# Performance work log

Hardware: AMD Instinct MI355X
Metric: run time of the kernel (lower is better)

The kernel has to match this reference:

```python
import jax, jax.numpy as jnp
import numpy as np
from jax import lax

B, L, D = 8, 2048, 512
K = 16            # cysteines per sequence (fixed by construction)
CYS = 4           # AA2ID['C']
CW = 5            # disulfide_context_window
KW = 2 * CW + 1   # conv kernel size = 11
H = D // 2        # LSTM hidden per direction = 256
STR = 0.4         # cys_optimization_strength


def setup_inputs() -> dict:
    key = jax.random.key(0)
    ks = jax.random.split(key, 16)
    hidden_states = jax.random.normal(ks[0], (B, L, D), jnp.float32)
    # amino-acid ids with exactly K cysteines per sequence, spaced > KW apart
    aa = jax.random.randint(ks[1], (B, L), 0, 20)
    aa = jnp.where(aa == CYS, 5, aa)
    base = 64 + 128 * jnp.arange(K)
    jitter = jax.random.randint(ks[2], (B, K), -40, 41)
    pos = base[None, :] + jitter  # [B,K], strictly increasing, gaps > 11
    aa_ids = aa.at[jnp.arange(B)[:, None], pos].set(CYS)
    s = 0.05
    W_bil = jax.random.normal(ks[3], (128, D, D)) * s
    b_bil = jax.random.normal(ks[4], (128,)) * s
    cls_w1 = jax.random.normal(ks[5], (64, 128)) * s
    cls_b1 = jax.random.normal(ks[6], (64,)) * s
    cls_w2 = jax.random.normal(ks[7], (1, 64)) * s
    cls_b2 = jax.random.normal(ks[8], (1,)) * s
    # 2 layers x 2 directions; both layers have input size D (2*H == D)
    lstm_Wih = jax.random.normal(ks[9], (2, 2, 4 * H, D)) * s
    lstm_Whh = jax.random.normal(ks[10], (2, 2, 4 * H, H)) * s
    lstm_bih = jax.random.normal(ks[11], (2, 2, 4 * H)) * s
    lstm_bhh = jax.random.normal(ks[12], (2, 2, 4 * H)) * s
    conv_w = jax.random.normal(ks[13], (D, D, KW)) * 0.02
    conv_b = jax.random.normal(ks[14], (D,)) * 0.02
    dsb_factor = jax.random.normal(ks[15], (D,)) * 0.1
    return dict(hidden_states=hidden_states, aa_ids=aa_ids, W_bil=W_bil,
                b_bil=b_bil, cls_w1=cls_w1, cls_b1=cls_b1, cls_w2=cls_w2,
                cls_b2=cls_b2, lstm_Wih=lstm_Wih, lstm_Whh=lstm_Whh,
                lstm_bih=lstm_bih, lstm_bhh=lstm_bhh, conv_w=conv_w,
                conv_b=conv_b, dsb_factor=dsb_factor)


def _lstm_dir(x, Wih, Whh, bih, bhh, reverse):
    # x: [B,L,In] -> [B,L,H]; PyTorch gate order i,f,g,o
    bsz = x.shape[0]
    xs = jnp.swapaxes(x, 0, 1)  # [L,B,In]
    if reverse:
        xs = xs[::-1]

    def step(carry, xt):
        h, c = carry
        g = xt @ Wih.T + h @ Whh.T + bih + bhh  # [B,4H]
        i, f, gg, o = jnp.split(g, 4, axis=-1)
        c = jax.nn.sigmoid(f) * c + jax.nn.sigmoid(i) * jnp.tanh(gg)
        h = jax.nn.sigmoid(o) * jnp.tanh(c)
        return (h, c), h

    init = (jnp.zeros((bsz, H), x.dtype), jnp.zeros((bsz, H), x.dtype))
    _, hs = lax.scan(step, init, xs)
    if reverse:
        hs = hs[::-1]
    return jnp.swapaxes(hs, 0, 1)


def _bilstm(x, Wih, Whh, bih, bhh):
    out = x
    for layer in range(2):  # dropout inactive in eval mode
        fw = _lstm_dir(out, Wih[layer, 0], Whh[layer, 0], bih[layer, 0], bhh[layer, 0], False)
        bw = _lstm_dir(out, Wih[layer, 1], Whh[layer, 1], bih[layer, 1], bhh[layer, 1], True)
        out = jnp.concatenate([fw, bw], axis=-1)
    return out


def reference(hidden_states, aa_ids, W_bil, b_bil, cls_w1, cls_b1, cls_w2,
              cls_b2, lstm_Wih, lstm_Whh, lstm_bih, lstm_bhh, conv_w, conv_b,
              dsb_factor):
    dt = hidden_states.dtype
    cys_mask = (aa_ids == CYS)  # [B,L] bool, exactly K per row
    pos = jax.vmap(lambda m: jnp.nonzero(m, size=K, fill_value=0)[0])(cys_mask)  # [B,K]

    # ---- batched bilinear + classifier over all cys pairs ----
    feats = jnp.take_along_axis(hidden_states, pos[:, :, None], axis=1)  # [B,K,D]
    t = jnp.einsum('bkd,cde->bkce', feats, W_bil)            # [B,K,128,D]
    pf = jnp.einsum('bkce,bme->bkmc', t, feats) + b_bil      # [B,K,K,128]
    h1 = jax.nn.relu(pf @ cls_w1.T + cls_b1)
    prob = jax.nn.sigmoid(h1 @ cls_w2.T + cls_b2)[..., 0]    # [B,K,K]
    dist = jnp.abs(pos[:, :, None] - pos[:, None, :])
    prob = jnp.where(dist < 2, prob * 0.1, prob)

    # ---- greedy NMS-style pair selection (prob desc, prob > 0.5, no reuse) ----
    iu, ju = jnp.triu_indices(K, k=1)  # P = K*(K-1)/2 pairs
    probs_flat = prob[:, iu, ju]       # [B,P]

    def greedy(pflat):
        order = jnp.argsort(-pflat)
        ii, jj, pp = iu[order], ju[order], pflat[order]

        def step(used, trip):
            i, j, p = trip
            sel = jnp.logical_and(jnp.logical_and(~used[i], ~used[j]), p > 0.5)
            used = used.at[i].set(used[i] | sel)
            used = used.at[j].set(used[j] | sel)
            return used, sel

        _, sels = lax.scan(step, jnp.zeros(K, bool), (ii, jj, pp))
        return jnp.zeros(iu.shape[0], bool).at[order].set(sels)

    sel_flat = jax.vmap(greedy)(probs_flat)
    sel_mat = jnp.zeros((B, K, K), bool).at[:, iu, ju].set(sel_flat)

    # ---- redox LSTM + windowed cys enhancement ----
    opt = _bilstm(hidden_states, lstm_Wih, lstm_Whh, lstm_bih, lstm_bhh)  # [B,L,D]
    cm = cys_mask.astype(dt)
    cov = lax.conv_general_dilated(cm[:, None, :], jnp.ones((1, 1, KW), dt),
                                   (1,), ((CW, CW),),
                                   dimension_numbers=('NCH', 'OIH', 'NCH'))[:, 0, :]
    win = (cov > 0).astype(dt)  # [B,L] 1 where within CW of a cysteine
    cys_enh = hidden_states + STR * opt * win[..., None] + dsb_factor * cm[..., None]

    # ---- local structure conv ----
    struct = lax.conv_general_dilated(jnp.swapaxes(cys_enh, 1, 2), conv_w,
                                      (1,), ((CW, CW),),
                                      dimension_numbers=('NCH', 'OIH', 'NCH'))
    struct = jnp.swapaxes(struct + conv_b[None, :, None], 1, 2)

    output = hidden_states + 0.3 * (cys_enh - hidden_states) + 0.2 * (struct - hidden_states)
    return (output, prob, sel_mat)
```

## Files before the change

### kernel.cpp

```cpp
#include <hip/hip_runtime.h>
#include <hip/hip_bf16.h>

typedef float  f32x4 __attribute__((ext_vector_type(4)));
typedef float  f32x2 __attribute__((ext_vector_type(2)));
typedef int    i32x4 __attribute__((ext_vector_type(4)));
typedef int    i32x8 __attribute__((ext_vector_type(8)));

#define NB   8
#define LSEQ 2048
#define DDIM 512
#define KC   16

__device__ __forceinline__ float rcp_(float x){ return __builtin_amdgcn_rcpf(x); }
__device__ __forceinline__ float ex2_(float x){ return __builtin_amdgcn_exp2f(x); }
__device__ __forceinline__ float clamp60(float x){ return fminf(fmaxf(x, -60.f), 60.f); }
__device__ __forceinline__ unsigned pk2(float a, float b){
    __hip_bfloat16 x=__float2bfloat16(a), y=__float2bfloat16(b);
    return (unsigned)*(unsigned short*)&x | ((unsigned)*(unsigned short*)&y<<16);
}

#define GLDS(gp, lp) __builtin_amdgcn_global_load_lds(                      \
    (__attribute__((address_space(1))) const void*)(gp),                   \
    (__attribute__((address_space(3))) void*)(lp), 16, 0, 0)

__global__ __launch_bounds__(256) void k_prep(const float* __restrict__ hidden, __hip_bfloat16* __restrict__ hbf,
                                              const float* __restrict__ Wih, __hip_bfloat16* __restrict__ wihbf,
                                              const float* __restrict__ bih, const float* __restrict__ bhh,
                                              float* __restrict__ bias2,
                                              const float* __restrict__ convw, __hip_bfloat16* __restrict__ wtc,
                                              const int* __restrict__ aa, int* __restrict__ pos,
                                              float* __restrict__ cm, float* __restrict__ win){
    int bid = blockIdx.x, tid = threadIdx.x;
    if(bid < 4096){
        size_t i = (size_t)bid*256 + tid;
        const f32x4* s = (const f32x4*)(hidden + i*8);
        f32x4 v0 = s[0], v1 = s[1];
        i32x4 o; o.x = pk2(v0.x,v0.y); o.y = pk2(v0.z,v0.w);
                 o.z = pk2(v1.x,v1.y); o.w = pk2(v1.z,v1.w);
        ((i32x4*)hbf)[i] = o;
    } else if(bid < 5120){
        size_t i = (size_t)(bid-4096)*256 + tid;
        const f32x4* s = (const f32x4*)(Wih + i*8);
        f32x4 v0 = s[0], v1 = s[1];
        i32x4 o; o.x = pk2(v0.x,v0.y); o.y = pk2(v0.z,v0.w);
                 o.z = pk2(v1.x,v1.y); o.w = pk2(v1.z,v1.w);
        ((i32x4*)wihbf)[i] = o;
    } else if(bid < 5136){
        int i = (bid-5120)*256 + tid;
        bias2[i] = bih[i] + bhh[i];
    } else if(bid < 6160){
        int idx = (bid-5136)*256 + tid;
        #pragma unroll
        for(int tap=0; tap<11; ++tap)
            wtc[(size_t)tap*262144 + idx] = __float2bfloat16(convw[(size_t)idx*11 + tap]);
    } else {
        int b = bid - 6160;
        __shared__ unsigned char fl[LSEQ];
        for(int t=tid; t<LSEQ; t+=256) fl[t] = (aa[b*LSEQ+t]==4) ? 1 : 0;
        __syncthreads();
        if(tid==0){
            int c=0;
            for(int t=0; t<LSEQ && c<KC; ++t) if(fl[t]) pos[b*KC + c++] = t;
            for(; c<KC; ++c) pos[b*KC+c]=0;
        }
        for(int t=tid; t<LSEQ; t+=256){
            cm[b*LSEQ+t] = fl[t] ? 1.f : 0.f;
            int lo = t-5 < 0 ? 0 : t-5;
            int hi = t+5 > LSEQ-1 ? LSEQ-1 : t+5;
            float wv = 0.f;
            for(int u=lo; u<=hi; ++u) if(fl[u]) wv = 1.f;
            win[b*LSEQ+t] = wv;
        }
    }
}

__global__ __launch_bounds__(256) void k_gemm(const __hip_bfloat16* __restrict__ A, const __hip_bfloat16* __restrict__ Bw,
                                              const float* __restrict__ bias, __hip_bfloat16* __restrict__ C,
                                              int N, int KD){
    int nt = blockIdx.x, mt = blockIdx.y;
    __shared__ __hip_bfloat16 As[128][32];
    __shared__ __hip_bfloat16 Bs[128][32];
    int tid = threadIdx.x, w = tid>>6, lane = tid&63, lo = lane&15, hi = lane>>4;
    int wm = w>>1, wn = w&1;
    f32x4 acc[4][4];
    #pragma unroll
    for(int s=0;s<4;s++){
        #pragma unroll
        for(int t2=0;t2<4;t2++) acc[s][t2] = (f32x4){0.f,0.f,0.f,0.f};
    }
    int lr = lane>>2, lc = (lane&3)*8;
    const __hip_bfloat16* Ab = A  + (size_t)(mt*128)*KD;
    const __hip_bfloat16* Bb = Bw + (size_t)(nt*128)*KD;
    for(int kk=0; kk<KD; kk+=32){
        __builtin_amdgcn_s_barrier();
        GLDS(Ab + (size_t)(w*32    + lr)*KD + kk + lc, &As[w*32   ][0]);
        GLDS(Ab + (size_t)(w*32+16 + lr)*KD + kk + lc, &As[w*32+16][0]);
        GLDS(Bb + (size_t)(w*32    + lr)*KD + kk + lc, &Bs[w*32   ][0]);
        GLDS(Bb + (size_t)(w*32+16 + lr)*KD + kk + lc, &Bs[w*32+16][0]);
        asm volatile("s_waitcnt vmcnt(0)" ::: "memory");
        __builtin_amdgcn_s_barrier();
        i32x4 av[4], bv[4];
        #pragma unroll
        for(int s=0;s<4;s++) av[s] = *(const i32x4*)(&As[wm*64+s*16+lo][hi*8]);
        #pragma unroll
        for(int t2=0;t2<4;t2++) bv[t2] = *(const i32x4*)(&Bs[wn*64+t2*16+lo][hi*8]);
        asm volatile("s_nop 1" ::);
        #pragma unroll
        for(int s=0;s<4;s++){
            #pragma unroll
            for(int t2=0;t2<4;t2++)
                asm volatile("v_mfma_f32_16x16x32_bf16 %0, %1, %2, %0" : "+v"(acc[s][t2]) : "v"(av[s]), "v"(bv[t2]));
        }
    }
    asm volatile("s_nop 7\n\ts_nop 7" ::);
    #pragma unroll
    for(int t2=0;t2<4;t2++){
        int n = nt*128 + wn*64 + t2*16 + lo;
        float bn = bias[n];
        #pragma unroll
        for(int s=0;s<4;s++){
            #pragma unroll
            for(int rr=0;rr<4;rr++){
                int m = mt*128 + wm*64 + s*16 + hi*4 + rr;
                C[(size_t)m*N + n] = __float2bfloat16(acc[s][t2][rr] + bn);
            }
        }
    }
}

__device__ __forceinline__ void recur_body(char* smem, const float* __restrict__ Whh,
        const __hip_bfloat16* __restrict__ Gx, __hip_bfloat16* __restrict__ Hout,
        int layer, int bat, int dir){
    unsigned char (*hb)[256]   = (unsigned char(*)[256])smem;
    __hip_bfloat16 (*gxs)[1024] = (__hip_bfloat16(*)[1024])(smem+512);
    const int tid = threadIdx.x, w = tid>>6, lane = tid&63, lo = lane&15, hi = lane>>4;
    for(int i=tid; i<128; i+=512) ((int*)smem)[i] = 0;

    i32x8 bf[8][2];
    const float* wbase = Whh + ((size_t)(layer*2 + dir)*1024)*256;
    #pragma unroll
    for(int q=0;q<4;q++){
        #pragma unroll
        for(int s=0;s<2;s++){
            int j = q*256 + w*32 + s*16 + lo;
            const float* wr = wbase + (size_t)j*256;
            #pragma unroll
            for(int c=0;c<2;c++){
                i32x8 v;
                #pragma unroll
                for(int u=0; u<8; ++u){
                    f32x4 wv = *(const f32x4*)(wr + c*128 + hi*32 + u*4);
                    int pk = __builtin_amdgcn_cvt_pk_fp8_f32(wv.x, wv.y, 0, false);
                    pk = __builtin_amdgcn_cvt_pk_fp8_f32(wv.z, wv.w, pk, true);
                    v[u] = pk;
                }
                bf[q*2+s][c] = v;
            }
        }
    }
    const int pm = w*32 + ((hi&1)<<4) + lo;
    float cst = 0.f;
    const __hip_bfloat16* gxbase = Gx + (size_t)bat*LSEQ*2048 + dir*1024;

    {
        int tok0 = dir ? (LSEQ-1) : 0;
        int tok1 = dir ? (LSEQ-2) : 1;
        if(w < 2){
            GLDS(gxbase + (size_t)tok0*2048 + w*512 + lane*8, &gxs[0][w*512]);
            GLDS(gxbase + (size_t)tok1*2048 + w*512 + lane*8, &gxs[1][w*512]);
        }
    }
    asm volatile("s_waitcnt vmcnt(1) lgkmcnt(0)" ::: "memory");
    __builtin_amdgcn_s_barrier();
    __builtin_amdgcn_sched_barrier(0);

    int cur = 0;
    for(int t=0; t<LSEQ; ++t){
        const int tt = dir ? (LSEQ-1-t) : t;
        const int hcur = t&1, hnxt = hcur^1;
        int nx2 = cur+2; if(nx2>=3) nx2-=3;
        {
            int tp = (t+2 < LSEQ) ? (t+2) : (LSEQ-1);
            int tok = dir ? (LSEQ-1-tp) : tp;
            if(w < 2) GLDS(gxbase + (size_t)tok*2048 + w*512 + lane*8, &gxs[nx2][w*512]);
        }
        i32x8 af[2];
        #pragma unroll
        for(int c=0;c<2;c++){
            i32x4 v0 = *(const i32x4*)(&hb[hcur][c*128 + hi*32]);
            i32x4 v1 = *(const i32x4*)(&hb[hcur][c*128 + hi*32 + 16]);
            af[c] = __builtin_shufflevector(v0, v1, 0,1,2,3,4,5,6,7);
        }
        f32x4 acc[8];
        #pragma unroll
        for(int i=0;i<8;i++) acc[i] = (f32x4){0.f,0.f,0.f,0.f};
        asm volatile("s_nop 1" ::);
        #pragma unroll
        for(int c=0;c<2;c++){
            #pragma unroll
            for(int i=0;i<8;i++)
                asm volatile("v_mfma_f32_16x16x128_f8f6f4 %0, %1, %2, %0"
                             : "+v"(acc[i]) : "v"(af[c]), "a"(bf[i][c]));
        }
        asm volatile("s_nop 7\n\ts_nop 7\n\ts_nop 7" ::);
        {
            float aI = (hi&1) ? acc[1][0] : acc[0][0];
            float aF = (hi&1) ? acc[3][0] : acc[2][0];
            float aG = (hi&1) ? acc[5][0] : acc[4][0];
            float aO = (hi&1) ? acc[7][0] : acc[6][0];
            float gi = aI + __bfloat162float(gxs[cur][      pm]);
            float gf = aF + __bfloat162float(gxs[cur][256 + pm]);
            float gg = aG + __bfloat162float(gxs[cur][512 + pm]);
            float go = aO + __bfloat162float(gxs[cur][768 + pm]);
            float sf = rcp_(1.f + ex2_(gf * -1.44269504f));
            float ag = ex2_(clamp60(gg * 2.88539008f));
            float bi = ex2_(clamp60(gi * -1.44269504f));
            float it = (ag - 1.f) * rcp_((1.f + bi) * (ag + 1.f));
            float c  = sf*cst + it;
            cst = c;
            float ac = ex2_(clamp60(c * 2.88539008f));
            float bo = ex2_(clamp60(go * -1.44269504f));
            float h  = (ac - 1.f) * rcp_((1.f + bo) * (ac + 1.f));
            if(hi < 2){
                int pk = __builtin_amdgcn_cvt_pk_fp8_f32(h, h, 0, false);
                hb[hnxt][pm] = (unsigned char)(pk & 0xff);
                Hout[((size_t)bat*LSEQ + tt)*512 + dir*256 + pm] = __float2bfloat16(h);
            }
        }
        asm volatile("s_waitcnt vmcnt(2) lgkmcnt(0)" ::: "memory");
        __builtin_amdgcn_s_barrier();
        __builtin_amdgcn_sched_barrier(0);
        cur = (cur+1 == 3) ? 0 : cur+1;
    }
}

__device__ __forceinline__ void bilinear_body(char* smem, const float* __restrict__ hidden,
        const int* __restrict__ pos, const float* __restrict__ Wb, const float* __restrict__ bb,
        float* __restrict__ pf, int idx){
    int c = idx & 127, b = idx >> 7;
    float (*fl)[516] = (float(*)[516])smem;
    float (*tl)[516] = (float(*)[516])(smem + 33024);
    int tid = threadIdx.x;
    for(int i=tid; i<2048; i+=512){
        int k = i>>7, d = (i&127)*4;
        int p = pos[b*KC + k];
        f32x4 v = *(const f32x4*)(hidden + ((size_t)b*LSEQ + p)*DDIM + d);
        fl[k][d]=v.x; fl[k][d+1]=v.y; fl[k][d+2]=v.z; fl[k][d+3]=v.w;
    }
    __syncthreads();
    int e = tid;
    float acc[16];
    #pragma unroll
    for(int k=0;k<16;k++) acc[k]=0.f;
    const float* wc = Wb + (size_t)c*512*512;
    for(int d=0; d<512; ++d){
        float wv = wc[(size_t)d*512 + e];
        #pragma unroll
        for(int k=0;k<16;k++) acc[k] += fl[k][d]*wv;
    }
    #pragma unroll
    for(int k=0;k<16;k++) tl[k][e] = acc[k];
    __syncthreads();
    if(tid < 256){
        int kq = tid>>4, mq = tid&15;
        const f32x4* tp = (const f32x4*)&tl[kq][0];
        const f32x4* fp = (const f32x4*)&fl[mq][0];
        float s = 0.f;
        #pragma unroll 8
        for(int e2=0;e2<128;e2++){ f32x4 a=tp[e2], v=fp[e2]; s += a.x*v.x + a.y*v.y + a.z*v.z + a.w*v.w; }
        pf[(((size_t)b*16+kq)*16+mq)*128 + c] = s + bb[c];
    }
}

__device__ __forceinline__ void clsgreedy_body(char* smem, const float* __restrict__ pf,
        const float* __restrict__ w1, const float* __restrict__ b1,
        const float* __restrict__ w2, const float* __restrict__ b2,
        const int* __restrict__ pos, float* __restrict__ prob, float* __restrict__ sel, int b){
    float (*sw1)[128] = (float(*)[128])smem;
    float* sw2 = (float*)(smem + 32768);
    float* sb1 = sw2 + 64;
    float* sp  = sb1 + 64;
    unsigned char* si = (unsigned char*)(sp + 120);
    unsigned char* sj = si + 120;
    int tid = threadIdx.x;
    for(int i=tid; i<8192; i+=512) sw1[i>>7][i&127] = w1[i];
    if(tid<64){ sw2[tid]=w2[tid]; sb1[tid]=b1[tid]; }
    if(tid==0){
        int idx=0;
        for(int i=0;i<16;i++) for(int j=i+1;j<16;j++){ si[idx]=(unsigned char)i; sj[idx]=(unsigned char)j; idx++; }
    }
    if(tid<256) sel[b*256+tid] = 0.f;
    __syncthreads();
    if(tid < 256){
        int k = tid>>4, m = tid&15;
        const f32x4* pp = (const f32x4*)(pf + (((size_t)b*16+k)*16+m)*128);
        f32x4 pr[32];
        #pragma unroll
        for(int i=0;i<32;i++) pr[i] = pp[i];
        float lg = b2[0];
        for(int n=0;n<64;n++){
            const f32x4* wr = (const f32x4*)&sw1[n][0];
            float a = sb1[n];
            #pragma unroll
            for(int i=0;i<32;i++){ f32x4 wv = wr[i]; a += pr[i].x*wv.x + pr[i].y*wv.y + pr[i].z*wv.z + pr[i].w*wv.w; }
            a = fmaxf(a, 0.f);
            lg += a*sw2[n];
        }
        float p = rcp_(1.f + ex2_(lg * -1.44269504f));
        int dk = pos[b*16+k]-pos[b*16+m]; if(dk<0) dk=-dk;
        if(dk<2) p *= 0.1f;
        prob[b*256 + k*16 + m] = p;
        if(k < m) sp[k*(31-k)/2 + (m-k-1)] = p;
    }
    __syncthreads();
    if(tid==0){
        bool done[120]; bool used[16];
        for(int i=0;i<120;i++) done[i]=false;
        for(int i=0;i<16;i++)  used[i]=false;
        for(int it=0; it<120; ++it){
            int bi=-1; float bp=-1e30f;
            for(int q=0;q<120;q++) if(!done[q] && sp[q]>bp){ bp=sp[q]; bi=q; }
            done[bi]=true;
            if(bp>0.5f && !used[si[bi]] && !used[sj[bi]]){
                used[si[bi]]=true; used[sj[bi]]=true;
                sel[b*256 + si[bi]*16 + sj[bi]] = 1.f;
            }
        }
    }
}

__global__ __launch_bounds__(512) void k_fused1(const float* __restrict__ Whh, const __hip_bfloat16* __restrict__ Gx,
        __hip_bfloat16* __restrict__ Hout,
        const float* __restrict__ hidden, const int* __restrict__ pos,
        const float* __restrict__ Wbil, const float* __restrict__ bbil, float* __restrict__ pf){
    __shared__ __attribute__((aligned(16))) char smem[98304];
    if(blockIdx.x < 16){
        recur_body(smem, Whh, Gx, Hout, 0, blockIdx.x>>1, blockIdx.x&1);
    } else {
        bilinear_body(smem, hidden, pos, Wbil, bbil, pf, blockIdx.x - 16);
    }
}

__global__ __launch_bounds__(512) void k_fused2(const float* __restrict__ Whh, const __hip_bfloat16* __restrict__ Gx,
        __hip_bfloat16* __restrict__ Hout,
        const float* __restrict__ pf, const float* __restrict__ w1, const float* __restrict__ b1,
        const float* __restrict__ w2, const float* __restrict__ b2, const int* __restrict__ pos,
        float* __restrict__ prob, float* __restrict__ sel){
    __shared__ __attribute__((aligned(16))) char smem[98304];
    if(blockIdx.x < 16){
        recur_body(smem, Whh, Gx, Hout, 1, blockIdx.x>>1, blockIdx.x&1);
    } else {
        clsgreedy_body(smem, pf, w1, b1, w2, b2, pos, prob, sel, blockIdx.x - 16);
    }
}

__global__ __launch_bounds__(256) void k_convce(const float* __restrict__ hs, const __hip_bfloat16* __restrict__ opt,
        const float* __restrict__ win, const float* __restrict__ cm, const float* __restrict__ dsb,
        const __hip_bfloat16* __restrict__ wt, const float* __restrict__ convb, float* __restrict__ outp){
    int mt = blockIdx.x & 31, b = blockIdx.x >> 5;
    __shared__ __hip_bfloat16 S[74][520];
    int tid = threadIdx.x;
    for(int i=tid; i<74*64; i+=256){
        int rq = i>>6, cc = (i&63)*8;
        int tok = mt*64 - 5 + rq;
        i32x4 o = (i32x4){0,0,0,0};
        if(tok>=0 && tok<LSEQ){
            size_t base = ((size_t)b*LSEQ + tok)*512 + cc;
            float wv = win[b*LSEQ+tok]*0.4f, cv = cm[b*LSEQ+tok];
            f32x4 h0 = *(const f32x4*)(hs + base);
            f32x4 h1 = *(const f32x4*)(hs + base + 4);
            unsigned long long u0 = *(const unsigned long long*)(opt + base);
            unsigned long long u1 = *(const unsigned long long*)(opt + base + 4);
            f32x4 d0 = *(const f32x4*)(dsb + cc);
            f32x4 d1 = *(const f32x4*)(dsb + cc + 4);
            float c0 = h0.x + wv*__uint_as_float((unsigned)(u0      & 0xffffull)<<16) + d0.x*cv;
            float c1 = h0.y + wv*__uint_as_float((unsigned)((u0>>16)& 0xffffull)<<16) + d0.y*cv;
            float c2 = h0.z + wv*__uint_as_float((unsigned)((u0>>32)& 0xffffull)<<16) + d0.z*cv;
            float c3 = h0.w + wv*__uint_as_float((unsigned)((u0>>48)& 0xffffull)<<16) + d0.w*cv;
            float c4 = h1.x + wv*__uint_as_float((unsigned)(u1      & 0xffffull)<<16) + d1.x*cv;
            float c5 = h1.y + wv*__uint_as_float((unsigned)((u1>>16)& 0xffffull)<<16) + d1.y*cv;
            float c6 = h1.z + wv*__uint_as_float((unsigned)((u1>>32)& 0xffffull)<<16) + d1.z*cv;
            float c7 = h1.w + wv*__uint_as_float((unsigned)((u1>>48)& 0xffffull)<<16) + d1.w*cv;
            o.x = pk2(c0,c1); o.y = pk2(c2,c3); o.z = pk2(c4,c5); o.w = pk2(c6,c7);
        }
        *(i32x4*)(&S[rq][cc]) = o;
    }
    __syncthreads();
    int w = tid>>6, lane = tid&63, lo = lane&15, hi = lane>>4;
    f32x4 acc[4][8];
    #pragma unroll
    for(int ms=0;ms<4;ms++){
        #pragma unroll
        for(int s=0;s<8;s++) acc[ms][s] = (f32x4){0.f,0.f,0.f,0.f};
    }
    asm volatile("s_nop 1" ::);
    for(int tap=0; tap<11; ++tap){
        const __hip_bfloat16* wtp = wt + (size_t)tap*262144 + (size_t)(w*128)*512;
        for(int kk=0; kk<512; kk+=32){
            i32x4 a[4];
            #pragma unroll
            for(int ms=0;ms<4;ms++) a[ms] = *(const i32x4*)(&S[ms*16 + lo + tap][kk + hi*8]);
            #pragma unroll
            for(int s=0;s<8;s++){
                i32x4 bq = *(const i32x4*)(wtp + (size_t)(s*16 + lo)*512 + kk + hi*8);
                #pragma unroll
                for(int ms=0;ms<4;ms++)
                    asm volatile("v_mfma_f32_16x16x32_bf16 %0, %1, %2, %0" : "+v"(acc[ms][s]) : "v"(a[ms]), "v"(bq));
            }
        }
    }
    asm volatile("s_nop 7\n\ts_nop 7" ::);
    #pragma unroll
    for(int s=0;s<8;s++){
        int co = w*128 + s*16 + lo;
        float cb = convb[co];
        #pragma unroll
        for(int ms=0;ms<4;ms++){
            #pragma unroll
            for(int rr=0; rr<4; ++rr){
                int row = ms*16 + hi*4 + rr;
                int tok = mt*64 + row;
                size_t gi = ((size_t)b*LSEQ + tok)*512 + co;
                float h   = hs[gi];
                float cef = __bfloat162float(S[row + 5][co]);
                outp[gi] = 0.5f*h + 0.3f*cef + 0.2f*(acc[ms][s][rr] + cb);
            }
        }
    }
}

extern "C" void kernel_launch(void* const* d_in, const int* in_sizes, int n_in,
                              void* d_out, int out_size, void* d_ws, size_t ws_size,
                              hipStream_t stream)
{
    (void)in_sizes; (void)n_in; (void)out_size; (void)ws_size;
    const float* hidden = (const float*)d_in[0];
    const int*   aa     = (const int*)d_in[1];
    const float* Wbil   = (const float*)d_in[2];
    const float* bbil   = (const float*)d_in[3];
    const float* w1     = (const float*)d_in[4];
    const float* b1     = (const float*)d_in[5];
    const float* w2     = (const float*)d_in[6];
    const float* b2     = (const float*)d_in[7];
    const float* Wih    = (const float*)d_in[8];
    const float* Whh    = (const float*)d_in[9];
    const float* bih    = (const float*)d_in[10];
    const float* bhh    = (const float*)d_in[11];
    const float* convw  = (const float*)d_in[12];
    const float* convb  = (const float*)d_in[13];
    const float* dsb    = (const float*)d_in[14];

    float* outp = (float*)d_out;
    float* prob = outp + (size_t)NB*LSEQ*DDIM;
    float* sel  = prob + NB*KC*KC;

    char* p = (char*)d_ws;
    auto alloc = [&](size_t bytes)->char*{ char* r = p; p += (bytes + 255) & ~(size_t)255; return r; };
    __hip_bfloat16* gx    = (__hip_bfloat16*)alloc((size_t)16384*2048*2);
    __hip_bfloat16* hbf   = (__hip_bfloat16*)alloc((size_t)NB*LSEQ*DDIM*2);
    __hip_bfloat16* wihbf = (__hip_bfloat16*)alloc((size_t)2*2048*512*2);
    float*          bias2 = (float*)        alloc((size_t)2*2048*4);
    __hip_bfloat16* out1  = (__hip_bfloat16*)alloc((size_t)NB*LSEQ*DDIM*2);
    __hip_bfloat16* out2  = (__hip_bfloat16*)alloc((size_t)NB*LSEQ*DDIM*2);
    __hip_bfloat16* wtc   = (__hip_bfloat16*)alloc((size_t)11*512*512*2);
    float*          pf    = (float*)        alloc((size_t)NB*KC*KC*128*4);
    int*            pos   = (int*)          alloc((size_t)NB*KC*4);
    float*          cm    = (float*)        alloc((size_t)NB*LSEQ*4);
    float*          win   = (float*)        alloc((size_t)NB*LSEQ*4);

    k_prep<<<6168, 256, 0, stream>>>(hidden, hbf, Wih, wihbf, bih, bhh, bias2, convw, wtc, aa, pos, cm, win);
    k_gemm<<<dim3(16, 128), 256, 0, stream>>>(hbf, wihbf, bias2, gx, 2048, 512);
    k_fused1<<<16 + 1024, 512, 0, stream>>>(Whh, gx, out1, hidden, pos, Wbil, bbil, pf);
    k_gemm<<<dim3(16, 128), 256, 0, stream>>>(out1, wihbf + (size_t)2048*512, bias2 + 2048, gx, 2048, 512);
    k_fused2<<<16 + 8, 512, 0, stream>>>(Whh, gx, out2, pf, w1, b1, w2, b2, pos, prob, sel);
    k_convce<<<256, 256, 0, stream>>>(hidden, out2, win, cm, dsb, wtc, convb, outp);
}
```

Baseline: 4.062 ms.

## Fuse input-projection GEMM into recurrence kernels with per-tile counter flags

The separate input-projection GEMM launches are folded into the fused LSTM kernels as extra blocks. Each GEMM block bumps an atomic counter per 128-token tile when it finishes, and the recurrence blocks spin on that counter before prefetching gate inputs. This lets the serial recurrence start while the projection is still being computed. GEMM tiles are ordered so that tiles near both sequence ends finish first, and the MFMA accumulation is split into two independent chains. The risks are deadlock if the recurrence blocks are not co-resident with enough GEMM blocks, and contention from spinning and the extra waits.

```diff
diff --git a/kernel.cpp b/kernel.cpp
--- a/kernel.cpp
+++ b/kernel.cpp
@@ -29,7 +29,8 @@
                                               float* __restrict__ bias2,
                                               const float* __restrict__ convw, __hip_bfloat16* __restrict__ wtc,
                                               const int* __restrict__ aa, int* __restrict__ pos,
-                                              float* __restrict__ cm, float* __restrict__ win){
+                                              float* __restrict__ cm, float* __restrict__ win,
+                                              int* __restrict__ cnt){
     int bid = blockIdx.x, tid = threadIdx.x;
     if(bid < 4096){
         size_t i = (size_t)bid*256 + tid;
@@ -53,7 +54,7 @@
         #pragma unroll
         for(int tap=0; tap<11; ++tap)
             wtc[(size_t)tap*262144 + idx] = __float2bfloat16(convw[(size_t)idx*11 + tap]);
-    } else {
+    } else if(bid < 6168){
         int b = bid - 6160;
         __shared__ unsigned char fl[LSEQ];
         for(int t=tid; t<LSEQ; t+=256) fl[t] = (aa[b*LSEQ+t]==4) ? 1 : 0;
@@ -71,42 +72,46 @@
             for(int u=lo; u<=hi; ++u) if(fl[u]) wv = 1.f;
             win[b*LSEQ+t] = wv;
         }
-    }
-}
-
-__global__ __launch_bounds__(256) void k_gemm(const __hip_bfloat16* __restrict__ A, const __hip_bfloat16* __restrict__ Bw,
-                                              const float* __restrict__ bias, __hip_bfloat16* __restrict__ C,
-                                              int N, int KD){
-    int nt = blockIdx.x, mt = blockIdx.y;
-    __shared__ __hip_bfloat16 As[128][32];
-    __shared__ __hip_bfloat16 Bs[128][32];
+    } else {
+        if(tid < 256) cnt[tid] = 0;
+    }
+}
+
+__device__ __forceinline__ void gemm_body(char* smem, const __hip_bfloat16* __restrict__ A,
+        const __hip_bfloat16* __restrict__ Bw, const float* __restrict__ bias,
+        __hip_bfloat16* __restrict__ C, int* __restrict__ cnt, int g){
+    const int KD = 512, N = 2048;
+    int nt = g & 15;
+    int j  = g >> 4;
+    int kpos = j >> 3, bat = j & 7;
+    int mt = bat*16 + ((kpos&1) ? (15 - (kpos>>1)) : (kpos>>1));
+    __hip_bfloat16 (*As)[32] = (__hip_bfloat16(*)[32])smem;
+    __hip_bfloat16 (*Bs)[32] = (__hip_bfloat16(*)[32])(smem + 8192);
     int tid = threadIdx.x, w = tid>>6, lane = tid&63, lo = lane&15, hi = lane>>4;
     int wm = w>>1, wn = w&1;
-    f32x4 acc[4][4];
-    #pragma unroll
-    for(int s=0;s<4;s++){
+    f32x4 acc[2][4];
+    #pragma unroll
+    for(int s=0;s<2;s++){
         #pragma unroll
         for(int t2=0;t2<4;t2++) acc[s][t2] = (f32x4){0.f,0.f,0.f,0.f};
     }
-    int lr = lane>>2, lc = (lane&3)*8;
+    int lr = tid>>2, lc = (tid&3)*8;
     const __hip_bfloat16* Ab = A  + (size_t)(mt*128)*KD;
     const __hip_bfloat16* Bb = Bw + (size_t)(nt*128)*KD;
     for(int kk=0; kk<KD; kk+=32){
         __builtin_amdgcn_s_barrier();
-        GLDS(Ab + (size_t)(w*32    + lr)*KD + kk + lc, &As[w*32   ][0]);
-        GLDS(Ab + (size_t)(w*32+16 + lr)*KD + kk + lc, &As[w*32+16][0]);
-        GLDS(Bb + (size_t)(w*32    + lr)*KD + kk + lc, &Bs[w*32   ][0]);
-        GLDS(Bb + (size_t)(w*32+16 + lr)*KD + kk + lc, &Bs[w*32+16][0]);
+        GLDS(Ab + (size_t)lr*KD + kk + lc, &As[lr][lc]);
+        GLDS(Bb + (size_t)lr*KD + kk + lc, &Bs[lr][lc]);
         asm volatile("s_waitcnt vmcnt(0)" ::: "memory");
         __builtin_amdgcn_s_barrier();
-        i32x4 av[4], bv[4];
-        #pragma unroll
-        for(int s=0;s<4;s++) av[s] = *(const i32x4*)(&As[wm*64+s*16+lo][hi*8]);
+        i32x4 av[2], bv[4];
+        #pragma unroll
+        for(int s=0;s<2;s++) av[s] = *(const i32x4*)(&As[wm*32+s*16+lo][hi*8]);
         #pragma unroll
         for(int t2=0;t2<4;t2++) bv[t2] = *(const i32x4*)(&Bs[wn*64+t2*16+lo][hi*8]);
         asm volatile("s_nop 1" ::);
         #pragma unroll
-        for(int s=0;s<4;s++){
+        for(int s=0;s<2;s++){
             #pragma unroll
             for(int t2=0;t2<4;t2++)
                 asm volatile("v_mfma_f32_16x16x32_bf16 %0, %1, %2, %0" : "+v"(acc[s][t2]) : "v"(av[s]), "v"(bv[t2]));
@@ -118,21 +123,25 @@
         int n = nt*128 + wn*64 + t2*16 + lo;
         float bn = bias[n];
         #pragma unroll
-        for(int s=0;s<4;s++){
+        for(int s=0;s<2;s++){
             #pragma unroll
             for(int rr=0;rr<4;rr++){
-                int m = mt*128 + wm*64 + s*16 + hi*4 + rr;
+                int m = mt*128 + wm*32 + s*16 + hi*4 + rr;
                 C[(size_t)m*N + n] = __float2bfloat16(acc[s][t2][rr] + bn);
             }
         }
     }
+    asm volatile("s_waitcnt vmcnt(0)" ::: "memory");
+    __syncthreads();
+    if(tid==0)
+        __hip_atomic_fetch_add(cnt + mt, 1, __ATOMIC_RELEASE, __HIP_MEMORY_SCOPE_AGENT);
 }
 
 __device__ __forceinline__ void recur_body(char* smem, const float* __restrict__ Whh,
         const __hip_bfloat16* __restrict__ Gx, __hip_bfloat16* __restrict__ Hout,
-        int layer, int bat, int dir){
-    unsigned char (*hb)[256]   = (unsigned char(*)[256])smem;
-    __hip_bfloat16 (*gxs)[1024] = (__hip_bfloat16(*)[1024])(smem+512);
+        const int* __restrict__ cnt, int layer, int bat, int dir){
+    unsigned char (*hb)[256]    = (unsigned char(*)[256])smem;
+    __hip_bfloat16 (*gxs)[1024] = (__hip_bfloat16(*)[1024])(smem + 512);
     const int tid = threadIdx.x, w = tid>>6, lane = tid&63, lo = lane&15, hi = lane>>4;
     for(int i=tid; i<128; i+=512) ((int*)smem)[i] = 0;
 
@@ -161,16 +170,24 @@
     const int pm = w*32 + ((hi&1)<<4) + lo;
     float cst = 0.f;
     const __hip_bfloat16* gxbase = Gx + (size_t)bat*LSEQ*2048 + dir*1024;
+    const int cbase = bat*16;
+    int mtr = -1;
 
     {
         int tok0 = dir ? (LSEQ-1) : 0;
         int tok1 = dir ? (LSEQ-2) : 1;
         if(w < 2){
+            int mtn = cbase + (tok0>>7);
+            if(lane==0){
+                while(__hip_atomic_load(cnt+mtn, __ATOMIC_ACQUIRE, __HIP_MEMORY_SCOPE_AGENT) < 16)
+                    __builtin_amdgcn_s_sleep(2);
+            }
+            mtr = mtn;
             GLDS(gxbase + (size_t)tok0*2048 + w*512 + lane*8, &gxs[0][w*512]);
             GLDS(gxbase + (size_t)tok1*2048 + w*512 + lane*8, &gxs[1][w*512]);
         }
     }
-    asm volatile("s_waitcnt vmcnt(1) lgkmcnt(0)" ::: "memory");
+    asm volatile("s_waitcnt vmcnt(0) lgkmcnt(0)" ::: "memory");
     __builtin_amdgcn_s_barrier();
     __builtin_amdgcn_sched_barrier(0);
 
@@ -179,10 +196,24 @@
         const int tt = dir ? (LSEQ-1-t) : t;
         const int hcur = t&1, hnxt = hcur^1;
         int nx2 = cur+2; if(nx2>=3) nx2-=3;
+        float xi = __bfloat162float(gxs[cur][      pm]);
+        float xf = __bfloat162float(gxs[cur][256 + pm]);
+        float xg = __bfloat162float(gxs[cur][512 + pm]);
+        float xo = __bfloat162float(gxs[cur][768 + pm]);
         {
             int tp = (t+2 < LSEQ) ? (t+2) : (LSEQ-1);
             int tok = dir ? (LSEQ-1-tp) : tp;
-            if(w < 2) GLDS(gxbase + (size_t)tok*2048 + w*512 + lane*8, &gxs[nx2][w*512]);
+            if(w < 2){
+                int mtn = cbase + (tok>>7);
+                if(mtn != mtr){
+                    if(lane==0){
+                        while(__hip_atomic_load(cnt+mtn, __ATOMIC_ACQUIRE, __HIP_MEMORY_SCOPE_AGENT) < 16)
+                            __builtin_amdgcn_s_sleep(2);
+                    }
+                    mtr = mtn;
+                }
+                GLDS(gxbase + (size_t)tok*2048 + w*512 + lane*8, &gxs[nx2][w*512]);
+            }
         }
         i32x8 af[2];
         #pragma unroll
@@ -191,27 +222,28 @@
             i32x4 v1 = *(const i32x4*)(&hb[hcur][c*128 + hi*32 + 16]);
             af[c] = __builtin_shufflevector(v0, v1, 0,1,2,3,4,5,6,7);
         }
-        f32x4 acc[8];
-        #pragma unroll
-        for(int i=0;i<8;i++) acc[i] = (f32x4){0.f,0.f,0.f,0.f};
+        f32x4 aa[8], ab[8];
+        #pragma unroll
+        for(int i=0;i<8;i++){ aa[i] = (f32x4){0.f,0.f,0.f,0.f}; ab[i] = (f32x4){0.f,0.f,0.f,0.f}; }
         asm volatile("s_nop 1" ::);
         #pragma unroll
-        for(int c=0;c<2;c++){
-            #pragma unroll
-            for(int i=0;i<8;i++)
-                asm volatile("v_mfma_f32_16x16x128_f8f6f4 %0, %1, %2, %0"
-                             : "+v"(acc[i]) : "v"(af[c]), "a"(bf[i][c]));
-        }
-        asm volatile("s_nop 7\n\ts_nop 7\n\ts_nop 7" ::);
+        for(int i=0;i<8;i++)
+            asm volatile("v_mfma_f32_16x16x128_f8f6f4 %0, %1, %2, %0"
+                         : "+v"(aa[i]) : "v"(af[0]), "a"(bf[i][0]));
+        #pragma unroll
+        for(int i=0;i<8;i++)
+            asm volatile("v_mfma_f32_16x16x128_f8f6f4 %0, %1, %2, %0"
+                         : "+v"(ab[i]) : "v"(af[1]), "a"(bf[i][1]));
+        asm volatile("s_nop 7\n\ts_nop 7" ::);
         {
-            float aI = (hi&1) ? acc[1][0] : acc[0][0];
-            float aF = (hi&1) ? acc[3][0] : acc[2][0];
-            float aG = (hi&1) ? acc[5][0] : acc[4][0];
-            float aO = (hi&1) ? acc[7][0] : acc[6][0];
-            float gi = aI + __bfloat162float(gxs[cur][      pm]);
-            float gf = aF + __bfloat162float(gxs[cur][256 + pm]);
-            float gg = aG + __bfloat162float(gxs[cur][512 + pm]);
-            float go = aO + __bfloat162float(gxs[cur][768 + pm]);
+            float aI = (hi&1) ? (aa[1][0]+ab[1][0]) : (aa[0][0]+ab[0][0]);
+            float aF = (hi&1) ? (aa[3][0]+ab[3][0]) : (aa[2][0]+ab[2][0]);
+            float aG = (hi&1) ? (aa[5][0]+ab[5][0]) : (aa[4][0]+ab[4][0]);
+            float aO = (hi&1) ? (aa[7][0]+ab[7][0]) : (aa[6][0]+ab[6][0]);
+            float gi = aI + xi;
+            float gf = aF + xf;
+            float gg = aG + xg;
+            float go = aO + xo;
             float sf = rcp_(1.f + ex2_(gf * -1.44269504f));
             float ag = ex2_(clamp60(gg * 2.88539008f));
             float bi = ex2_(clamp60(gi * -1.44269504f));
@@ -329,28 +361,38 @@
     }
 }
 
-__global__ __launch_bounds__(512) void k_fused1(const float* __restrict__ Whh, const __hip_bfloat16* __restrict__ Gx,
-        __hip_bfloat16* __restrict__ Hout,
+__global__ __launch_bounds__(512) void k_fused1(const float* __restrict__ Whh, __hip_bfloat16* __restrict__ Gx,
+        __hip_bfloat16* __restrict__ Hout, int* __restrict__ cnt,
+        const __hip_bfloat16* __restrict__ hbf, const __hip_bfloat16* __restrict__ wihbf,
+        const float* __restrict__ bias2,
         const float* __restrict__ hidden, const int* __restrict__ pos,
         const float* __restrict__ Wbil, const float* __restrict__ bbil, float* __restrict__ pf){
     __shared__ __attribute__((aligned(16))) char smem[98304];
-    if(blockIdx.x < 16){
-        recur_body(smem, Whh, Gx, Hout, 0, blockIdx.x>>1, blockIdx.x&1);
+    int bid = blockIdx.x;
+    if(bid < 16){
+        recur_body(smem, Whh, Gx, Hout, cnt, 0, bid>>1, bid&1);
+    } else if(bid < 16 + 2048){
+        gemm_body(smem, hbf, wihbf, bias2, Gx, cnt, bid - 16);
     } else {
-        bilinear_body(smem, hidden, pos, Wbil, bbil, pf, blockIdx.x - 16);
-    }
-}
-
-__global__ __launch_bounds__(512) void k_fused2(const float* __restrict__ Whh, const __hip_bfloat16* __restrict__ Gx,
-        __hip_bfloat16* __restrict__ Hout,
+        bilinear_body(smem, hidden, pos, Wbil, bbil, pf, bid - 2064);
+    }
+}
+
+__global__ __launch_bounds__(512) void k_fused2(const float* __restrict__ Whh, __hip_bfloat16* __restrict__ Gx,
+        __hip_bfloat16* __restrict__ Hout, int* __restrict__ cnt,
+        const __hip_bfloat16* __restrict__ out1, const __hip_bfloat16* __restrict__ wihbf,
+        const float* __restrict__ bias2,
         const float* __restrict__ pf, const float* __restrict__ w1, const float* __restrict__ b1,
         const float* __restrict__ w2, const float* __restrict__ b2, const int* __restrict__ pos,
         float* __restrict__ prob, float* __restrict__ sel){
     __shared__ __attribute__((aligned(16))) char smem[98304];
-    if(blockIdx.x < 16){
-        recur_body(smem, Whh, Gx, Hout, 1, blockIdx.x>>1, blockIdx.x&1);
+    int bid = blockIdx.x;
+    if(bid < 16){
+        recur_body(smem, Whh, Gx, Hout, cnt, 1, bid>>1, bid&1);
+    } else if(bid < 16 + 2048){
+        gemm_body(smem, out1, wihbf + (size_t)2048*512, bias2 + 2048, Gx, cnt, bid - 16);
     } else {
-        clsgreedy_body(smem, pf, w1, b1, w2, b2, pos, prob, sel, blockIdx.x - 16);
+        clsgreedy_body(smem, pf, w1, b1, w2, b2, pos, prob, sel, bid - 2064);
     }
 }
 
@@ -467,11 +509,13 @@
     int*            pos   = (int*)          alloc((size_t)NB*KC*4);
     float*          cm    = (float*)        alloc((size_t)NB*LSEQ*4);
     float*          win   = (float*)        alloc((size_t)NB*LSEQ*4);
-
-    k_prep<<<6168, 256, 0, stream>>>(hidden, hbf, Wih, wihbf, bih, bhh, bias2, convw, wtc, aa, pos, cm, win);
-    k_gemm<<<dim3(16, 128), 256, 0, stream>>>(hbf, wihbf, bias2, gx, 2048, 512);
-    k_fused1<<<16 + 1024, 512, 0, stream>>>(Whh, gx, out1, hidden, pos, Wbil, bbil, pf);
-    k_gemm<<<dim3(16, 128), 256, 0, stream>>>(out1, wihbf + (size_t)2048*512, bias2 + 2048, gx, 2048, 512);
-    k_fused2<<<16 + 8, 512, 0, stream>>>(Whh, gx, out2, pf, w1, b1, w2, b2, pos, prob, sel);
+    int*            cnt1  = (int*)          alloc((size_t)256*4);
+    int*            cnt2  = cnt1 + 128;
+
+    k_prep<<<6169, 256, 0, stream>>>(hidden, hbf, Wih, wihbf, bih, bhh, bias2, convw, wtc, aa, pos, cm, win, cnt1);
+    k_fused1<<<16 + 2048 + 1024, 512, 0, stream>>>(Whh, gx, out1, cnt1, hbf, wihbf, bias2,
+                                                   hidden, pos, Wbil, bbil, pf);
+    k_fused2<<<16 + 2048 + 8, 512, 0, stream>>>(Whh, gx, out2, cnt2, out1, wihbf, bias2,
+                                                pf, w1, b1, w2, b2, pos, prob, sel);
     k_convce<<<256, 256, 0, stream>>>(hidden, out2, win, cm, dsb, wtc, convb, outp);
 }
```

Result: no change. 4.067 ms (+0.1%).
